# Kernel optimization log

Hardware: AMD Instinct MI355X
Metric: run time of the kernel (lower is better)

## Reference

```python
import jax, jax.numpy as jnp
import numpy as np

D_MODEL = 1024
DK = 64
N_HEADS = D_MODEL // DK
MASK = True


def setup_inputs() -> dict:
    key = jax.random.key(0)
    ks = jax.random.split(key, 8)
    B, S = 4, 2048
    scale = 1.0 / np.sqrt(D_MODEL)
    return {
        "query_data": jax.random.normal(ks[0], (B, S, D_MODEL), dtype=jnp.float32),
        "key_data": jax.random.normal(ks[1], (B, S, D_MODEL), dtype=jnp.float32),
        "value_data": jax.random.normal(ks[2], (B, S, D_MODEL), dtype=jnp.float32),
        "Wq": jax.random.normal(ks[3], (D_MODEL, D_MODEL), dtype=jnp.float32) * scale,
        "Wk": jax.random.normal(ks[4], (D_MODEL, D_MODEL), dtype=jnp.float32) * scale,
        "Wv": jax.random.normal(ks[5], (D_MODEL, D_MODEL), dtype=jnp.float32) * scale,
        "Wp": jax.random.normal(ks[6], (D_MODEL, D_MODEL), dtype=jnp.float32) * scale,
        "bp": jnp.zeros((D_MODEL,), dtype=jnp.float32),
    }


def reference(query_data, key_data, value_data, Wq, Wk, Wv, Wp, bp):
    B, S, _ = query_data.shape
    # QKV projections, split into heads: (B, H, S, dk)
    def split_heads(x, W):
        return (x @ W.T).reshape(B, -1, N_HEADS, DK).transpose(0, 2, 1, 3)

    q = split_heads(query_data, Wq)
    k = split_heads(key_data, Wk)
    v = split_heads(value_data, Wv)

    scores = jnp.einsum("bhqd,bhkd->bhqk", q, k) / np.sqrt(DK).astype(np.float32)
    if MASK:
        Sq, Sk = scores.shape[-2], scores.shape[-1]
        causal = jnp.triu(jnp.ones((Sq, Sk), dtype=scores.dtype), k=1) * jnp.float32(-1e13)
        scores = scores + causal  # broadcast over (B, H)
    attn = jax.nn.softmax(scores, axis=-1)
    out = jnp.einsum("bhqk,bhkd->bhqd", attn, v)
    out = out.transpose(0, 2, 1, 3).reshape(B, S, D_MODEL)
    # dropout is identity in eval mode
    return out @ Wp.T + bp
```

## Files before the change

### kernel.cpp

```cpp
#include <hip/hip_runtime.h>
#include <hip/hip_bf16.h>
#include <stdint.h>

#define D_MODEL 1024
#define SEQ     2048
#define BATCH   4
#define NH      16
#define DKK     64
#define MROWS   (BATCH * SEQ)

typedef unsigned short u16;
using bf16x8 = __attribute__((ext_vector_type(8))) __bf16;
using f32x4  = __attribute__((ext_vector_type(4))) float;

__device__ __forceinline__ u16 f2bf(float f) {
    union { float f; uint32_t u; } v; v.f = f;
    return (u16)((v.u + 0x7FFFu + ((v.u >> 16) & 1u)) >> 16);
}
__device__ __forceinline__ uint32_t pk2bf(float a, float b) {
    union { __hip_bfloat162 h; uint32_t u; } v;
    v.h = __float22bfloat162_rn(float2{a, b});
    return v.u;
}

__device__ __forceinline__ float fast_exp2(float x) {
    float r; asm("v_exp_f32 %0, %1" : "=v"(r) : "v"(x)); return r;
}
__device__ __forceinline__ float fast_rcp(float x) {
    float r; asm("v_rcp_f32 %0, %1" : "=v"(r) : "v"(x)); return r;
}

__device__ __forceinline__ void gl_lds16(const u16* g, u16* l) {
    __builtin_amdgcn_global_load_lds(
        (__attribute__((address_space(1))) void*)(const_cast<u16*>(g)),
        (__attribute__((address_space(3))) void*)l, 16, 0, 0);
}

__global__ __launch_bounds__(256) void cvt_all(const float* __restrict__ a,
                                               const float* __restrict__ b,
                                               const float* __restrict__ c,
                                               const float* __restrict__ w0,
                                               const float* __restrict__ w1,
                                               const float* __restrict__ w2,
                                               const float* __restrict__ w3,
                                               u16* __restrict__ da,
                                               u16* __restrict__ db,
                                               u16* __restrict__ dc,
                                               u16* __restrict__ dw0,
                                               u16* __restrict__ dw1,
                                               u16* __restrict__ dw2,
                                               u16* __restrict__ dw3) {
    const int i = blockIdx.x * 256 + threadIdx.x;
    const float* s;
    u16* d;
    int off;
    if (i < 3 * (1 << 21)) {
        const int sel = i >> 21;
        off = i & ((1 << 21) - 1);
        s = (sel == 0) ? a : (sel == 1) ? b : c;
        d = (sel == 0) ? da : (sel == 1) ? db : dc;
    } else {
        const int j = i - 3 * (1 << 21);
        const int sel = j >> 18;
        off = j & ((1 << 18) - 1);
        s = (sel == 0) ? w0 : (sel == 1) ? w1 : (sel == 2) ? w2 : w3;
        d = (sel == 0) ? dw0 : (sel == 1) ? dw1 : (sel == 2) ? dw2 : dw3;
    }
    float4 v = ((const float4*)s)[off];
    uint2 o;
    o.x = pk2bf(v.x, v.y); o.y = pk2bf(v.z, v.w);
    ((uint2*)d)[off] = o;
}

__global__ __launch_bounds__(256, 3) void gemm_qkv(const u16* __restrict__ XQ,
                                                   const u16* __restrict__ XK,
                                                   const u16* __restrict__ XV,
                                                   const u16* __restrict__ WQ,
                                                   const u16* __restrict__ WK,
                                                   const u16* __restrict__ WV,
                                                   u16* __restrict__ Qo,
                                                   u16* __restrict__ Ko,
                                                   u16* __restrict__ Vto) {
    constexpr int K = 1024, N = 1024;
    __shared__ __align__(16) u16 smem[17408];
    u16* ldsA = smem;
    u16* ldsB = smem + 8192;
    u16* ldsT = smem;

    const int which = blockIdx.x >> 9;
    const int inner = blockIdx.x & 511;
    const u16* A  = (which == 0) ? XQ : (which == 1) ? XK : XV;
    const u16* Bw = (which == 0) ? WQ : (which == 1) ? WK : WV;

    const int t = threadIdx.x;
    const int w = t >> 6, lane = t & 63;
    const int quad = lane >> 4, l15 = lane & 15;
    const int x = inner & 7, j = inner >> 3;
    const int bm = x * 8 + (j >> 3), bn = j & 7;
    const int wm = (w >> 1) * 64, wn = (w & 1) * 64;

    const u16* Ab = A  + (size_t)bm * 128 * K;
    const u16* Bb = Bw + (size_t)bn * 128 * K;
    const int srow  = lane >> 2;
    const int scol8 = (lane & 3) * 8;

    f32x4 acc[4][4];
    #pragma unroll
    for (int i = 0; i < 4; ++i)
        #pragma unroll
        for (int jj = 0; jj < 4; ++jj)
            acc[i][jj] = f32x4{0.f, 0.f, 0.f, 0.f};

    #pragma unroll
    for (int i = 0; i < 2; ++i) {
        const int c = w * 2 + i;
        gl_lds16(Ab + (size_t)(c * 16 + srow) * K + scol8, &ldsA[c * 512]);
        gl_lds16(Bb + (size_t)(c * 16 + srow) * K + scol8, &ldsB[c * 512]);
    }

    int cur = 0;
    for (int k0 = 0; k0 < K; k0 += 32) {
        __syncthreads();
        if (k0 + 32 < K) {
            const int nxt = cur ^ 1;
            #pragma unroll
            for (int i = 0; i < 2; ++i) {
                const int c = w * 2 + i;
                gl_lds16(Ab + (size_t)(c * 16 + srow) * K + k0 + 32 + scol8, &ldsA[nxt * 4096 + c * 512]);
                gl_lds16(Bb + (size_t)(c * 16 + srow) * K + k0 + 32 + scol8, &ldsB[nxt * 4096 + c * 512]);
            }
        }

        bf16x8 afr[4], bfr[4];
        #pragma unroll
        for (int i = 0; i < 4; ++i)
            afr[i] = *(const bf16x8*)&ldsA[cur * 4096 + (wm + i * 16 + l15) * 32 + quad * 8];
        #pragma unroll
        for (int jj = 0; jj < 4; ++jj)
            bfr[jj] = *(const bf16x8*)&ldsB[cur * 4096 + (wn + jj * 16 + l15) * 32 + quad * 8];

        #pragma unroll
        for (int i = 0; i < 4; ++i)
            #pragma unroll
            for (int jj = 0; jj < 4; ++jj)
                acc[i][jj] = __builtin_amdgcn_mfma_f32_16x16x32_bf16(afr[i], bfr[jj], acc[i][jj], 0, 0, 0);
        cur ^= 1;
    }

    if (which < 2) {
        u16* outb = which ? Ko : Qo;
        #pragma unroll
        for (int i = 0; i < 4; ++i)
            #pragma unroll
            for (int jj = 0; jj < 4; ++jj)
                #pragma unroll
                for (int r = 0; r < 4; ++r) {
                    const int row = bm * 128 + wm + i * 16 + quad * 4 + r;
                    const int col = bn * 128 + wn + jj * 16 + l15;
                    outb[(size_t)row * N + col] = f2bf(acc[i][jj][r]);
                }
    } else {
        __syncthreads();
        #pragma unroll
        for (int i = 0; i < 4; ++i)
            #pragma unroll
            for (int jj = 0; jj < 4; ++jj)
                #pragma unroll
                for (int r = 0; r < 4; ++r) {
                    const int row_l = wm + i * 16 + quad * 4 + r;
                    const int col_l = wn + jj * 16 + l15;
                    ldsT[col_l * 136 + row_l] = f2bf(acc[i][jj][r]);
                }
        __syncthreads();
        const int c = t >> 1, half = t & 1;
        const int colg = bn * 128 + c;
        const int hh = colg >> 6, dd = colg & 63;
        const int bb = bm >> 4;
        const int s0 = ((bm * 128) & 2047) + half * 64;
        const u16* srcl = ldsT + c * 136 + half * 64;
        u16* dstg = Vto + (size_t)((bb * NH + hh) * DKK + dd) * SEQ + s0;
        #pragma unroll
        for (int k = 0; k < 8; ++k)
            *(uint4*)(dstg + k * 8) = *(const uint4*)(srcl + k * 8);
    }
}

__global__ __launch_bounds__(256, 3) void gemm_proj(const u16* __restrict__ A,
                                                    const u16* __restrict__ Bw,
                                                    float* __restrict__ outf,
                                                    const float* __restrict__ bias) {
    constexpr int K = 1024, N = 1024;
    __shared__ __align__(16) u16 ldsA[2 * 4096];
    __shared__ __align__(16) u16 ldsB[2 * 4096];

    const int t = threadIdx.x;
    const int w = t >> 6, lane = t & 63;
    const int quad = lane >> 4, l15 = lane & 15;
    const int x = blockIdx.x & 7, j = blockIdx.x >> 3;
    const int bm = x * 8 + ((j & 63) >> 3), bn = j & 7;
    const int wm = (w >> 1) * 64, wn = (w & 1) * 64;

    const u16* Ab = A  + (size_t)bm * 128 * K;
    const u16* Bb = Bw + (size_t)bn * 128 * K;
    const int srow  = lane >> 2;
    const int scol8 = (lane & 3) * 8;

    f32x4 acc[4][4];
    #pragma unroll
    for (int i = 0; i < 4; ++i)
        #pragma unroll
        for (int jj = 0; jj < 4; ++jj)
            acc[i][jj] = f32x4{0.f, 0.f, 0.f, 0.f};

    #pragma unroll
    for (int i = 0; i < 2; ++i) {
        const int c = w * 2 + i;
        gl_lds16(Ab + (size_t)(c * 16 + srow) * K + scol8, &ldsA[c * 512]);
        gl_lds16(Bb + (size_t)(c * 16 + srow) * K + scol8, &ldsB[c * 512]);
    }

    int cur = 0;
    for (int k0 = 0; k0 < K; k0 += 32) {
        __syncthreads();
        if (k0 + 32 < K) {
            const int nxt = cur ^ 1;
            #pragma unroll
            for (int i = 0; i < 2; ++i) {
                const int c = w * 2 + i;
                gl_lds16(Ab + (size_t)(c * 16 + srow) * K + k0 + 32 + scol8, &ldsA[nxt * 4096 + c * 512]);
                gl_lds16(Bb + (size_t)(c * 16 + srow) * K + k0 + 32 + scol8, &ldsB[nxt * 4096 + c * 512]);
            }
        }

        bf16x8 afr[4], bfr[4];
        #pragma unroll
        for (int i = 0; i < 4; ++i)
            afr[i] = *(const bf16x8*)&ldsA[cur * 4096 + (wm + i * 16 + l15) * 32 + quad * 8];
        #pragma unroll
        for (int jj = 0; jj < 4; ++jj)
            bfr[jj] = *(const bf16x8*)&ldsB[cur * 4096 + (wn + jj * 16 + l15) * 32 + quad * 8];

        #pragma unroll
        for (int i = 0; i < 4; ++i)
            #pragma unroll
            for (int jj = 0; jj < 4; ++jj)
                acc[i][jj] = __builtin_amdgcn_mfma_f32_16x16x32_bf16(afr[i], bfr[jj], acc[i][jj], 0, 0, 0);
        cur ^= 1;
    }

    #pragma unroll
    for (int i = 0; i < 4; ++i)
        #pragma unroll
        for (int jj = 0; jj < 4; ++jj)
            #pragma unroll
            for (int r = 0; r < 4; ++r) {
                const int row = bm * 128 + wm + i * 16 + quad * 4 + r;
                const int col = bn * 128 + wn + jj * 16 + l15;
                outf[(size_t)row * N + col] = acc[i][jj][r] + bias[col];
            }
}

__global__ __launch_bounds__(256, 4) void flash_attn(const u16* __restrict__ Qb,
                                                     const u16* __restrict__ Kb,
                                                     const u16* __restrict__ Vt,
                                                     u16* __restrict__ O) {
    __shared__ __align__(16) u16 ldsK[2 * 4096];
    __shared__ __align__(16) u16 ldsV[2 * 4096];

    const int t = threadIdx.x;
    const int w = t >> 6, lane = t & 63;
    const int quad = lane >> 4, l15 = lane & 15;
    const int bh = blockIdx.x & 63;
    const int qt = 15 - (blockIdx.x >> 6);
    const int b = bh >> 4, h = bh & 15;
    const int qw = qt * 128 + w * 32;

    const int s0own = (lane >> 4) & 1;
    const int srcA  = ((lane & 16) << 1) | ((lane & 32) >> 1) | l15;
    const int srcB  = srcA ^ 16;
    const bool hi5  = (lane & 32) != 0;

    const int srow  = lane >> 2;
    const int scol8 = (lane & 3) * 8;
    const size_t kbase = (size_t)b * SEQ * D_MODEL + h * DKK;
    const size_t vbase = (size_t)(bh * DKK) * SEQ;

    const float C2 = 0.18033688f;

    union { bf16x8 v; uint32_t u[4]; } onesf;
    #pragma unroll
    for (int i = 0; i < 4; ++i) onesf.u[i] = 0x3F803F80u;

    bf16x8 qf[2][2];
    #pragma unroll
    for (int g = 0; g < 2; ++g) {
        const u16* Qrow = Qb + (size_t)(b * SEQ + qw + g * 16 + l15) * D_MODEL + h * DKK;
        qf[g][0] = *(const bf16x8*)(Qrow + quad * 8);
        qf[g][1] = *(const bf16x8*)(Qrow + 32 + quad * 8);
    }

    f32x4 o_acc[2][4], o_l[2];
    #pragma unroll
    for (int g = 0; g < 2; ++g) {
        o_l[g] = f32x4{0.f, 0.f, 0.f, 0.f};
        #pragma unroll
        for (int nt = 0; nt < 4; ++nt) o_acc[g][nt] = f32x4{0.f, 0.f, 0.f, 0.f};
    }

    const int ntiles = 2 * qt + 2;

    #pragma unroll
    for (int i = 0; i < 2; ++i) {
        const int e = w * 2 + i, ch = e >> 2, rb = (e & 3) * 16;
        gl_lds16(Kb + kbase + (size_t)(rb + srow) * D_MODEL + ch * 32 + scol8,
                 &ldsK[ch * 2048 + rb * 32]);
        gl_lds16(Vt + vbase + (size_t)(rb + srow) * SEQ + ch * 32 + scol8,
                 &ldsV[ch * 2048 + rb * 32]);
    }

    int cur = 0;
    for (int it = 0; it < ntiles; ++it) {
        const int kb = it * 64;
        __syncthreads();

        if (it + 1 < ntiles) {
            const int nb = kb + 64, nxt = cur ^ 1;
            #pragma unroll
            for (int i = 0; i < 2; ++i) {
                const int e = w * 2 + i, ch = e >> 2, rb = (e & 3) * 16;
                gl_lds16(Kb + kbase + (size_t)(nb + rb + srow) * D_MODEL + ch * 32 + scol8,
                         &ldsK[nxt * 4096 + ch * 2048 + rb * 32]);
                gl_lds16(Vt + vbase + (size_t)(rb + srow) * SEQ + nb + ch * 32 + scol8,
                         &ldsV[nxt * 4096 + ch * 2048 + rb * 32]);
            }
        }

        if (kb <= qw + 31) {
            f32x4 sc[2][4];
            #pragma unroll
            for (int g = 0; g < 2; ++g)
                #pragma unroll
                for (int jt = 0; jt < 4; ++jt) sc[g][jt] = f32x4{0.f, 0.f, 0.f, 0.f};
            __builtin_amdgcn_s_setprio(1);
            #pragma unroll
            for (int ks = 0; ks < 2; ++ks)
                #pragma unroll
                for (int jt = 0; jt < 4; ++jt) {
                    bf16x8 kf = *(const bf16x8*)&ldsK[cur * 4096 + ks * 2048 + (jt * 16 + l15) * 32 + quad * 8];
                    #pragma unroll
                    for (int g = 0; g < 2; ++g)
                        sc[g][jt] = __builtin_amdgcn_mfma_f32_16x16x32_bf16(kf, qf[g][ks], sc[g][jt], 0, 0, 0);
                }
            __builtin_amdgcn_s_setprio(0);

            if (kb + 63 >= qw) {
                #pragma unroll
                for (int g = 0; g < 2; ++g)
                    #pragma unroll
                    for (int jt = 0; jt < 4; ++jt)
                        #pragma unroll
                        for (int r = 0; r < 4; ++r)
                            if (kb + jt * 16 + quad * 4 + r > qw + g * 16 + l15) sc[g][jt][r] = -3.0e38f;
            }

            uint32_t pw[2][4][2];
            #pragma unroll
            for (int g = 0; g < 2; ++g) {
                #pragma unroll
                for (int jt = 0; jt < 4; ++jt) {
                    float p[4];
                    #pragma unroll
                    for (int r = 0; r < 4; ++r)
                        p[r] = fast_exp2(sc[g][jt][r] * C2);
                    pw[g][jt][0] = pk2bf(p[0], p[1]);
                    pw[g][jt][1] = pk2bf(p[2], p[3]);
                }
            }

            #pragma unroll
            for (int ks = 0; ks < 2; ++ks) {
                union { bf16x8 v; uint32_t u[4]; } pa[2];
                #pragma unroll
                for (int g = 0; g < 2; ++g) {
                    uint32_t r1[2], r2[2];
                    #pragma unroll
                    for (int i = 0; i < 2; ++i) {
                        const uint32_t a = pw[g][2 * ks][i];
                        const uint32_t bb2 = pw[g][2 * ks + 1][i];
                        r1[i] = (uint32_t)__builtin_amdgcn_ds_bpermute(srcA << 2, (int)(s0own ? bb2 : a));
                        r2[i] = (uint32_t)__builtin_amdgcn_ds_bpermute(srcB << 2, (int)(s0own ? a : bb2));
                    }
                    pa[g].u[0] = hi5 ? r2[0] : r1[0];
                    pa[g].u[1] = hi5 ? r2[1] : r1[1];
                    pa[g].u[2] = hi5 ? r1[0] : r2[0];
                    pa[g].u[3] = hi5 ? r1[1] : r2[1];
                }
                __builtin_amdgcn_s_setprio(1);
                #pragma unroll
                for (int nt = 0; nt < 4; ++nt) {
                    bf16x8 vf = *(const bf16x8*)&ldsV[cur * 4096 + ks * 2048 + (nt * 16 + l15) * 32 + quad * 8];
                    #pragma unroll
                    for (int g = 0; g < 2; ++g)
                        o_acc[g][nt] = __builtin_amdgcn_mfma_f32_16x16x32_bf16(pa[g].v, vf, o_acc[g][nt], 0, 0, 0);
                }
                #pragma unroll
                for (int g = 0; g < 2; ++g)
                    o_l[g] = __builtin_amdgcn_mfma_f32_16x16x32_bf16(pa[g].v, onesf.v, o_l[g], 0, 0, 0);
                __builtin_amdgcn_s_setprio(0);
            }
        }

        cur ^= 1;
    }

    #pragma unroll
    for (int g = 0; g < 2; ++g) {
        float rl[4];
        #pragma unroll
        for (int r = 0; r < 4; ++r)
            rl[r] = fast_rcp(o_l[g][r]);
        #pragma unroll
        for (int nt = 0; nt < 4; ++nt)
            #pragma unroll
            for (int r = 0; r < 4; ++r) {
                const int qg = qw + g * 16 + quad * 4 + r;
                O[(size_t)(b * SEQ + qg) * D_MODEL + h * DKK + nt * 16 + l15] = f2bf(o_acc[g][nt][r] * rl[r]);
            }
    }
}

extern "C" void kernel_launch(void* const* d_in, const int* in_sizes, int n_in,
                              void* d_out, int out_size, void* d_ws, size_t ws_size,
                              hipStream_t stream) {
    const float* q_in = (const float*)d_in[0];
    const float* k_in = (const float*)d_in[1];
    const float* v_in = (const float*)d_in[2];
    const float* Wq   = (const float*)d_in[3];
    const float* Wk   = (const float*)d_in[4];
    const float* Wv   = (const float*)d_in[5];
    const float* Wp   = (const float*)d_in[6];
    const float* bp   = (const float*)d_in[7];
    float* out = (float*)d_out;

    char* ws = (char*)d_ws;
    u16* XQ  = (u16*)(ws + (size_t)0);
    u16* XK  = (u16*)(ws + ((size_t)16 << 20));
    u16* XV  = (u16*)(ws + ((size_t)32 << 20));
    u16* WQb = (u16*)(ws + ((size_t)48 << 20));
    u16* WKb = (u16*)(ws + ((size_t)50 << 20));
    u16* WVb = (u16*)(ws + ((size_t)52 << 20));
    u16* WPb = (u16*)(ws + ((size_t)54 << 20));
    u16* Qb  = (u16*)(ws + ((size_t)56 << 20));
    u16* Kb  = (u16*)(ws + ((size_t)72 << 20));
    u16* Vtb = (u16*)(ws + ((size_t)88 << 20));

    cvt_all<<<(3 * (1 << 21) + 4 * (1 << 18)) / 256, 256, 0, stream>>>(
        q_in, k_in, v_in, Wq, Wk, Wv, Wp,
        XQ, XK, XV, WQb, WKb, WVb, WPb);

    gemm_qkv<<<1536, 256, 0, stream>>>(XQ, XK, XV, WQb, WKb, WVb, Qb, Kb, Vtb);

    flash_attn<<<BATCH * NH * (SEQ / 128), 256, 0, stream>>>(Qb, Kb, Vtb, XQ);

    gemm_proj<<<512, 256, 0, stream>>>(XQ, WPb, out, bp);
}
```

Baseline: 300.8 us.

## Restructure QKV GEMM to 256x256 tiles with 8 waves and phased pipeline

```diff
diff --git a/kernel.cpp b/kernel.cpp
--- a/kernel.cpp
+++ b/kernel.cpp
@@ -35,6 +35,12 @@
         (__attribute__((address_space(1))) void*)(const_cast<u16*>(g)),
         (__attribute__((address_space(3))) void*)l, 16, 0, 0);
 }
+
+#define PIPE_BAR(VMC) do { \
+    asm volatile("s_waitcnt vmcnt(" VMC ")" ::: "memory"); \
+    __builtin_amdgcn_sched_barrier(0); \
+    __builtin_amdgcn_s_barrier(); \
+    __builtin_amdgcn_sched_barrier(0); } while (0)
 
 __global__ __launch_bounds__(256) void cvt_all(const float* __restrict__ a,
                                                const float* __restrict__ b,
@@ -72,7 +78,40 @@
     ((uint2*)d)[off] = o;
 }
 
-__global__ __launch_bounds__(256, 3) void gemm_qkv(const u16* __restrict__ XQ,
+template<int RH, int CH>
+__device__ __forceinline__ void gphase(const u16* ldsA, const u16* ldsB, int buf,
+                                       int wr, int wc, int quad, int l15, int xk,
+                                       f32x4 (&acc)[2][2][4][2]) {
+    bf16x8 af[4][2], bfr[2][2];
+    #pragma unroll
+    for (int i = 0; i < 4; ++i) {
+        const int row = RH * 128 + wr * 64 + i * 16 + l15;
+        #pragma unroll
+        for (int ks = 0; ks < 2; ++ks)
+            af[i][ks] = *(const bf16x8*)&ldsA[(buf << 14) + row * 64 +
+                                              ((((ks << 2) | quad) ^ xk) << 3)];
+    }
+    #pragma unroll
+    for (int j = 0; j < 2; ++j) {
+        const int col = CH * 128 + wc * 32 + j * 16 + l15;
+        #pragma unroll
+        for (int ks = 0; ks < 2; ++ks)
+            bfr[j][ks] = *(const bf16x8*)&ldsB[(buf << 14) + col * 64 +
+                                               ((((ks << 2) | quad) ^ xk) << 3)];
+    }
+    __builtin_amdgcn_s_setprio(1);
+    #pragma unroll
+    for (int i = 0; i < 4; ++i)
+        #pragma unroll
+        for (int j = 0; j < 2; ++j)
+            #pragma unroll
+            for (int ks = 0; ks < 2; ++ks)
+                acc[RH][CH][i][j] = __builtin_amdgcn_mfma_f32_16x16x32_bf16(
+                    af[i][ks], bfr[j][ks], acc[RH][CH][i][j], 0, 0, 0);
+    __builtin_amdgcn_s_setprio(0);
+}
+
+__global__ __launch_bounds__(512, 2) void gemm_qkv(const u16* __restrict__ XQ,
                                                    const u16* __restrict__ XK,
                                                    const u16* __restrict__ XV,
                                                    const u16* __restrict__ WQ,
@@ -82,106 +121,118 @@
                                                    u16* __restrict__ Ko,
                                                    u16* __restrict__ Vto) {
     constexpr int K = 1024, N = 1024;
-    __shared__ __align__(16) u16 smem[17408];
+    __shared__ __align__(16) u16 smem[65536];
     u16* ldsA = smem;
-    u16* ldsB = smem + 8192;
+    u16* ldsB = smem + 32768;
     u16* ldsT = smem;
 
-    const int which = blockIdx.x >> 9;
-    const int inner = blockIdx.x & 511;
+    const int which = blockIdx.x >> 7;
+    const int inner = blockIdx.x & 127;
+    const int bm = inner & 31, bn = inner >> 5;
     const u16* A  = (which == 0) ? XQ : (which == 1) ? XK : XV;
     const u16* Bw = (which == 0) ? WQ : (which == 1) ? WK : WV;
 
     const int t = threadIdx.x;
     const int w = t >> 6, lane = t & 63;
     const int quad = lane >> 4, l15 = lane & 15;
-    const int x = inner & 7, j = inner >> 3;
-    const int bm = x * 8 + (j >> 3), bn = j & 7;
-    const int wm = (w >> 1) * 64, wn = (w & 1) * 64;
-
-    const u16* Ab = A  + (size_t)bm * 128 * K;
-    const u16* Bb = Bw + (size_t)bn * 128 * K;
-    const int srow  = lane >> 2;
-    const int scol8 = (lane & 3) * 8;
-
-    f32x4 acc[4][4];
-    #pragma unroll
-    for (int i = 0; i < 4; ++i)
-        #pragma unroll
-        for (int jj = 0; jj < 4; ++jj)
-            acc[i][jj] = f32x4{0.f, 0.f, 0.f, 0.f};
-
-    #pragma unroll
-    for (int i = 0; i < 2; ++i) {
-        const int c = w * 2 + i;
-        gl_lds16(Ab + (size_t)(c * 16 + srow) * K + scol8, &ldsA[c * 512]);
-        gl_lds16(Bb + (size_t)(c * 16 + srow) * K + scol8, &ldsB[c * 512]);
-    }
-
-    int cur = 0;
-    for (int k0 = 0; k0 < K; k0 += 32) {
-        __syncthreads();
-        if (k0 + 32 < K) {
-            const int nxt = cur ^ 1;
-            #pragma unroll
-            for (int i = 0; i < 2; ++i) {
-                const int c = w * 2 + i;
-                gl_lds16(Ab + (size_t)(c * 16 + srow) * K + k0 + 32 + scol8, &ldsA[nxt * 4096 + c * 512]);
-                gl_lds16(Bb + (size_t)(c * 16 + srow) * K + k0 + 32 + scol8, &ldsB[nxt * 4096 + c * 512]);
-            }
-        }
-
-        bf16x8 afr[4], bfr[4];
-        #pragma unroll
-        for (int i = 0; i < 4; ++i)
-            afr[i] = *(const bf16x8*)&ldsA[cur * 4096 + (wm + i * 16 + l15) * 32 + quad * 8];
-        #pragma unroll
-        for (int jj = 0; jj < 4; ++jj)
-            bfr[jj] = *(const bf16x8*)&ldsB[cur * 4096 + (wn + jj * 16 + l15) * 32 + quad * 8];
-
-        #pragma unroll
-        for (int i = 0; i < 4; ++i)
-            #pragma unroll
-            for (int jj = 0; jj < 4; ++jj)
-                acc[i][jj] = __builtin_amdgcn_mfma_f32_16x16x32_bf16(afr[i], bfr[jj], acc[i][jj], 0, 0, 0);
-        cur ^= 1;
-    }
+    const int wr = w >> 2, wc = w & 3;
+    const int xk = l15 & 7;
+
+    const u16* Ab = A  + (size_t)bm * 256 * K;
+    const u16* Bb = Bw + (size_t)bn * 256 * K;
+
+    const int sr  = t >> 3;
+    const int scS = ((t & 7) ^ (sr & 7)) * 8;
+
+    auto stA = [&](int kt, int half) {
+        #pragma unroll
+        for (int i = 0; i < 2; ++i)
+            gl_lds16(Ab + (size_t)(half * 128 + i * 64 + sr) * K + kt * 64 + scS,
+                     &ldsA[((kt & 1) << 14) + (half * 128 + i * 64 + (w << 3)) * 64]);
+    };
+    auto stB = [&](int kt, int half) {
+        #pragma unroll
+        for (int i = 0; i < 2; ++i)
+            gl_lds16(Bb + (size_t)(half * 128 + i * 64 + sr) * K + kt * 64 + scS,
+                     &ldsB[((kt & 1) << 14) + (half * 128 + i * 64 + (w << 3)) * 64]);
+    };
+
+    f32x4 acc[2][2][4][2];
+    #pragma unroll
+    for (int rh = 0; rh < 2; ++rh)
+        #pragma unroll
+        for (int ch = 0; ch < 2; ++ch)
+            #pragma unroll
+            for (int i = 0; i < 4; ++i)
+                #pragma unroll
+                for (int j = 0; j < 2; ++j)
+                    acc[rh][ch][i][j] = f32x4{0.f, 0.f, 0.f, 0.f};
+
+    stA(0, 0); stB(0, 0); stA(0, 1); stB(0, 1); stA(1, 0); stB(1, 0);
+
+    for (int kt = 0; kt < 15; ++kt) {
+        const int buf = kt & 1;
+        PIPE_BAR("6"); stA(kt + 1, 1);
+        gphase<0, 0>(ldsA, ldsB, buf, wr, wc, quad, l15, xk, acc);
+        PIPE_BAR("6"); stB(kt + 1, 1);
+        gphase<0, 1>(ldsA, ldsB, buf, wr, wc, quad, l15, xk, acc);
+        PIPE_BAR("6"); if (kt < 14) stA(kt + 2, 0);
+        gphase<1, 0>(ldsA, ldsB, buf, wr, wc, quad, l15, xk, acc);
+        PIPE_BAR("6"); if (kt < 14) stB(kt + 2, 0);
+        gphase<1, 1>(ldsA, ldsB, buf, wr, wc, quad, l15, xk, acc);
+    }
+    PIPE_BAR("4");
+    gphase<0, 0>(ldsA, ldsB, 1, wr, wc, quad, l15, xk, acc);
+    PIPE_BAR("0");
+    gphase<0, 1>(ldsA, ldsB, 1, wr, wc, quad, l15, xk, acc);
+    gphase<1, 0>(ldsA, ldsB, 1, wr, wc, quad, l15, xk, acc);
+    gphase<1, 1>(ldsA, ldsB, 1, wr, wc, quad, l15, xk, acc);
 
     if (which < 2) {
         u16* outb = which ? Ko : Qo;
         #pragma unroll
-        for (int i = 0; i < 4; ++i)
-            #pragma unroll
-            for (int jj = 0; jj < 4; ++jj)
-                #pragma unroll
-                for (int r = 0; r < 4; ++r) {
-                    const int row = bm * 128 + wm + i * 16 + quad * 4 + r;
-                    const int col = bn * 128 + wn + jj * 16 + l15;
-                    outb[(size_t)row * N + col] = f2bf(acc[i][jj][r]);
-                }
+        for (int rh = 0; rh < 2; ++rh)
+            #pragma unroll
+            for (int ch = 0; ch < 2; ++ch)
+                #pragma unroll
+                for (int i = 0; i < 4; ++i)
+                    #pragma unroll
+                    for (int j = 0; j < 2; ++j)
+                        #pragma unroll
+                        for (int r = 0; r < 4; ++r) {
+                            const int row = bm * 256 + rh * 128 + wr * 64 + i * 16 + quad * 4 + r;
+                            const int col = bn * 256 + ch * 128 + wc * 32 + j * 16 + l15;
+                            outb[(size_t)row * N + col] = f2bf(acc[rh][ch][i][j][r]);
+                        }
     } else {
-        __syncthreads();
-        #pragma unroll
-        for (int i = 0; i < 4; ++i)
-            #pragma unroll
-            for (int jj = 0; jj < 4; ++jj)
-                #pragma unroll
-                for (int r = 0; r < 4; ++r) {
-                    const int row_l = wm + i * 16 + quad * 4 + r;
-                    const int col_l = wn + jj * 16 + l15;
-                    ldsT[col_l * 136 + row_l] = f2bf(acc[i][jj][r]);
-                }
-        __syncthreads();
-        const int c = t >> 1, half = t & 1;
-        const int colg = bn * 128 + c;
-        const int hh = colg >> 6, dd = colg & 63;
-        const int bb = bm >> 4;
-        const int s0 = ((bm * 128) & 2047) + half * 64;
-        const u16* srcl = ldsT + c * 136 + half * 64;
-        u16* dstg = Vto + (size_t)((bb * NH + hh) * DKK + dd) * SEQ + s0;
-        #pragma unroll
-        for (int k = 0; k < 8; ++k)
-            *(uint4*)(dstg + k * 8) = *(const uint4*)(srcl + k * 8);
+        #pragma unroll
+        for (int ch2 = 0; ch2 < 2; ++ch2) {
+            __syncthreads();
+            #pragma unroll
+            for (int rh = 0; rh < 2; ++rh)
+                #pragma unroll
+                for (int i = 0; i < 4; ++i)
+                    #pragma unroll
+                    for (int j = 0; j < 2; ++j)
+                        #pragma unroll
+                        for (int r = 0; r < 4; ++r) {
+                            const int row_l = rh * 128 + wr * 64 + i * 16 + quad * 4 + r;
+                            const int col_l = wc * 32 + j * 16 + l15;
+                            ldsT[col_l * 264 + row_l] =
+                                f2bf(ch2 ? acc[rh][1][i][j][r] : acc[rh][0][i][j][r]);
+                        }
+            __syncthreads();
+            const int c = t >> 2, qtr = t & 3;
+            const int colg = bn * 256 + ch2 * 128 + c;
+            const int hh = colg >> 6, dd = colg & 63;
+            const int bb = bm >> 3;
+            const int s0 = (bm & 7) * 256 + qtr * 64;
+            const u16* srcl = ldsT + c * 264 + qtr * 64;
+            u16* dstg = Vto + (size_t)((bb * NH + hh) * DKK + dd) * SEQ + s0;
+            #pragma unroll
+            for (int k = 0; k < 8; ++k)
+                *(uint4*)(dstg + k * 8) = *(const uint4*)(srcl + k * 8);
+        }
     }
 }
 
@@ -458,7 +509,7 @@
         q_in, k_in, v_in, Wq, Wk, Wv, Wp,
         XQ, XK, XV, WQb, WKb, WVb, WPb);
 
-    gemm_qkv<<<1536, 256, 0, stream>>>(XQ, XK, XV, WQb, WKb, WVb, Qb, Kb, Vtb);
+    gemm_qkv<<<384, 512, 0, stream>>>(XQ, XK, XV, WQb, WKb, WVb, Qb, Kb, Vtb);
 
     flash_attn<<<BATCH * NH * (SEQ / 128), 256, 0, stream>>>(Qb, Kb, Vtb, XQ);
 
```

Result: slower. 312.0 us (+3.7%).
